# Optimization experiments

Hardware: AMD Instinct MI355X
Metric: run time of the kernel (lower is better)

The kernel has to match this reference:

```python
import jax, jax.numpy as jnp
import numpy as np

INPUT_DIM = 6
HIDDEN = 256
NUM_CLASSES = 8
B = 16
V = 32768


def setup_inputs() -> dict:
    key = jax.random.key(0)
    ks = jax.random.split(key, 8)
    x = jax.random.normal(ks[0], (B, INPUT_DIM, V), dtype=jnp.float32)
    obj_idx = jax.random.randint(ks[1], (B,), 0, NUM_CLASSES)
    # Stacked per-class expert weights (Conv1d kernel_size=1 == pointwise linear)
    s1 = 1.0 / np.sqrt(INPUT_DIM)
    s2 = 1.0 / np.sqrt(HIDDEN)
    w1 = jax.random.uniform(ks[2], (NUM_CLASSES, HIDDEN, INPUT_DIM), jnp.float32, -s1, s1)
    b1 = jax.random.uniform(ks[3], (NUM_CLASSES, HIDDEN), jnp.float32, -s1, s1)
    w2 = jax.random.uniform(ks[4], (NUM_CLASSES, HIDDEN, HIDDEN), jnp.float32, -s2, s2)
    b2 = jax.random.uniform(ks[5], (NUM_CLASSES, HIDDEN), jnp.float32, -s2, s2)
    w3 = jax.random.uniform(ks[6], (NUM_CLASSES, 1, HIDDEN), jnp.float32, -s2, s2)
    b3 = jax.random.uniform(ks[7], (NUM_CLASSES, 1), jnp.float32, -s2, s2)
    return {"x": x, "obj_idx": obj_idx, "w1": w1, "b1": b1,
            "w2": w2, "b2": b2, "w3": w3, "b3": b3}


def reference(x, obj_idx, w1, b1, w2, b2, w3, b3):
    # Gather each sample's expert weights, then run the fused 3-layer pointwise
    # MLP over all B*V positions in one batched einsum per layer (no Python
    # loop over samples, unlike the original torch code).
    # x: [B, 6, V] -> out: [B, 1, V]
    h = jax.nn.relu(jnp.einsum('boi,biv->bov', w1[obj_idx], x) + b1[obj_idx][:, :, None])
    h = jax.nn.relu(jnp.einsum('boi,biv->bov', w2[obj_idx], h) + b2[obj_idx][:, :, None])
    out = jnp.einsum('boi,biv->bov', w3[obj_idx], h) + b3[obj_idx][:, :, None]
    return out
```

## Files before the change

kernel.cpp:

```cpp
#include <hip/hip_runtime.h>
#include <hip/hip_bf16.h>

typedef __bf16 bf16x8 __attribute__((ext_vector_type(8)));
typedef __bf16 bf16x4 __attribute__((ext_vector_type(4)));
typedef float  f32x4  __attribute__((ext_vector_type(4)));
typedef float  f32x16 __attribute__((ext_vector_type(16)));

#define V_TOTAL 32768
#define NT      512
#define NV      32
#define NBLK    256

#define W2_LDS  32768
#define H1_LDS  65536
#define RED_LDS 4096
#define LDS_TOT (W2_LDS + H1_LDS + RED_LDS)

#define GLOAD_LDS16(g, l) __builtin_amdgcn_global_load_lds( \
    (const __attribute__((address_space(1))) void*)(g),     \
    (__attribute__((address_space(3))) void*)(l), 16, 0, 0)

__global__ void w2_to_bf16(const float* __restrict__ w2, __bf16* __restrict__ w2b) {
    int i = blockIdx.x * 256 + threadIdx.x;
    int e = i >> 16, q = i & 65535;
    int c = q >> 9, w = q & 511, lane = w >> 3, j = w & 7;
    int ks = c >> 3, tile = c & 7;
    int m = tile * 32 + (lane & 31);
    int k = ks * 16 + (lane >> 5) * 8 + j;
    w2b[i] = (__bf16)w2[e * 65536 + m * 256 + k];
}

__global__ __launch_bounds__(NT) void fused_mlp(
    const float* __restrict__ x,  const int* __restrict__ obj,
    const float* __restrict__ w1, const float* __restrict__ b1,
    const float* __restrict__ b2, const float* __restrict__ w3,
    const float* __restrict__ b3, const __bf16* __restrict__ w2b,
    float* __restrict__ out)
{
    extern __shared__ __align__(16) char smem[];
    char*  w2s = smem;
    char*  h1t = smem + W2_LDS;
    float* red = (float*)(smem + W2_LDS + H1_LDS);

    const int t    = threadIdx.x;
    const int lane = t & 63;
    const int wv   = t >> 6;
    const int c32  = lane & 31;
    const int hh   = lane >> 5;
    const int b    = blockIdx.x >> 4;
    const int g    = blockIdx.x & 15;
    const int e    = __builtin_amdgcn_readfirstlane(obj[b]);
    const __bf16* w2sw = w2b + (size_t)e * 65536;

    #pragma unroll
    for (int it = 0; it < 4; ++it) {
        int c0 = it * 8 + wv;
        GLOAD_LDS16(w2sw + c0 * 512 + lane * 8, w2s + c0 * 1024);
    }

    bf16x8 aar[12];
    #pragma unroll
    for (int k2 = 0; k2 < 12; ++k2)
        aar[k2] = *(const bf16x8*)(w2sw + ((4 + k2) * 8 + wv) * 512 + lane * 8);

    const float* w1e = w1 + e * 1536;
    const float* b1e = b1 + e * 256;
    const float* b2e = b2 + e * 256;
    const float* w3e = w3 + e * 256;
    bf16x8 aa1 = {};
    if (hh == 0)
        #pragma unroll
        for (int j = 0; j < 6; ++j) aa1[j] = (__bf16)w1e[(wv * 32 + c32) * 6 + j];
    const float b3e = b3[e];
    const float* xe = x + (size_t)b * 6 * V_TOTAL;

    bf16x8 xf[2];
    auto load_x = [&](int ic) {
        #pragma unroll
        for (int pt = 0; pt < 2; ++pt) {
            bf16x8 v = {};
            #pragma unroll
            for (int i = 0; i < 6; ++i)
                v[i] = (__bf16)xe[i * V_TOTAL + (g * NV + ic) * 64 + pt * 32 + c32];
            xf[pt] = v;
        }
    };
    auto do_l1 = [&](int pan) {
        f32x16 b1f;
        #pragma unroll
        for (int gg = 0; gg < 4; ++gg) {
            f32x4 v = *(const f32x4*)(b1e + wv * 32 + gg * 8 + hh * 4);
            #pragma unroll
            for (int q = 0; q < 4; ++q) b1f[gg * 4 + q] = v[q];
        }
        #pragma unroll
        for (int pt = 0; pt < 2; ++pt) {
            f32x16 h = __builtin_amdgcn_mfma_f32_32x32x16_bf16(aa1, xf[pt], b1f, 0, 0, 0);
            #pragma unroll
            for (int gg = 0; gg < 4; ++gg) {
                bf16x4 pk;
                #pragma unroll
                for (int q = 0; q < 4; ++q) pk[q] = (__bf16)fmaxf(h[gg * 4 + q], 0.f);
                *(bf16x4*)(h1t + pan * 32768 + ((wv * 2 + (gg >> 1)) * 2 + pt) * 1024
                           + (gg & 1) * 512 + c32 * 16 + hh * 8) = pk;
            }
        }
    };

    load_x(0);
    do_l1(0);
    load_x(1);

    for (int iv = 0; iv < NV; ++iv) {
        __syncthreads();

        if (iv > 0 && t < 64) {
            const float* rq = red + ((iv - 1) & 1) * 512;
            float s = b3e;
            #pragma unroll
            for (int w8 = 0; w8 < 8; ++w8) s += rq[w8 * 64 + t];
            out[(size_t)b * V_TOTAL + (g * NV + iv - 1) * 64 + t] = s;
        }

        f32x16 acc0, acc1;
        #pragma unroll
        for (int gg = 0; gg < 4; ++gg) {
            f32x4 v = *(const f32x4*)(b2e + wv * 32 + gg * 8 + hh * 4);
            #pragma unroll
            for (int q = 0; q < 4; ++q) { acc0[gg * 4 + q] = v[q]; acc1[gg * 4 + q] = v[q]; }
        }
        const char* bbase = h1t + (iv & 1) * 32768 + lane * 16;
        #pragma unroll
        for (int ks = 0; ks < 4; ++ks) {
            const bf16x8 aw = *(const bf16x8*)(w2s + (ks * 8 + wv) * 1024 + lane * 16);
            const bf16x8 bb0 = *(const bf16x8*)(bbase + (ks * 2 + 0) * 1024);
            const bf16x8 bb1 = *(const bf16x8*)(bbase + (ks * 2 + 1) * 1024);
            acc0 = __builtin_amdgcn_mfma_f32_32x32x16_bf16(aw, bb0, acc0, 0, 0, 0);
            acc1 = __builtin_amdgcn_mfma_f32_32x32x16_bf16(aw, bb1, acc1, 0, 0, 0);
        }
        #pragma unroll
        for (int k2 = 0; k2 < 12; ++k2) {
            const bf16x8 bb0 = *(const bf16x8*)(bbase + ((4 + k2) * 2 + 0) * 1024);
            const bf16x8 bb1 = *(const bf16x8*)(bbase + ((4 + k2) * 2 + 1) * 1024);
            acc0 = __builtin_amdgcn_mfma_f32_32x32x16_bf16(aar[k2], bb0, acc0, 0, 0, 0);
            acc1 = __builtin_amdgcn_mfma_f32_32x32x16_bf16(aar[k2], bb1, acc1, 0, 0, 0);
        }

        float p0 = 0.f, p1 = 0.f;
        #pragma unroll
        for (int gg = 0; gg < 4; ++gg) {
            f32x4 wq = *(const f32x4*)(w3e + wv * 32 + gg * 8 + hh * 4);
            #pragma unroll
            for (int q = 0; q < 4; ++q) {
                p0 = fmaf(wq[q], fmaxf(acc0[gg * 4 + q], 0.f), p0);
                p1 = fmaf(wq[q], fmaxf(acc1[gg * 4 + q], 0.f), p1);
            }
        }
        p0 += __shfl_xor(p0, 32, 64);
        p1 += __shfl_xor(p1, 32, 64);
        float* rp = red + (iv & 1) * 512;
        if (lane < 32) {
            rp[wv * 64 + c32]      = p0;
            rp[wv * 64 + 32 + c32] = p1;
        }

        if (iv + 1 < NV) {
            do_l1((iv + 1) & 1);
            if (iv + 2 < NV) load_x(iv + 2);
        }
    }
    __syncthreads();
    if (t < 64) {
        const float* rq = red + ((NV - 1) & 1) * 512;
        float s = b3e;
        #pragma unroll
        for (int w8 = 0; w8 < 8; ++w8) s += rq[w8 * 64 + t];
        out[(size_t)b * V_TOTAL + (g * NV + NV - 1) * 64 + t] = s;
    }
}

extern "C" void kernel_launch(void* const* d_in, const int* in_sizes, int n_in,
                              void* d_out, int out_size, void* d_ws, size_t ws_size,
                              hipStream_t stream) {
    const float* x   = (const float*)d_in[0];
    const int*   obj = (const int*)d_in[1];
    const float* w1  = (const float*)d_in[2];
    const float* b1  = (const float*)d_in[3];
    const float* w2  = (const float*)d_in[4];
    const float* b2  = (const float*)d_in[5];
    const float* w3  = (const float*)d_in[6];
    const float* b3  = (const float*)d_in[7];
    float*  out = (float*)d_out;
    __bf16* w2b = (__bf16*)d_ws;

    (void)hipFuncSetAttribute((const void*)fused_mlp,
                              hipFuncAttributeMaxDynamicSharedMemorySize, LDS_TOT);

    w2_to_bf16<<<2048, 256, 0, stream>>>(w2, w2b);
    fused_mlp<<<NBLK, NT, LDS_TOT, stream>>>(x, obj, w1, b1, b2, w3, b3, w2b, out);
}
```

Baseline: 76.11 us.

## Add producer warps for layer-1 and move more W2 into LDS

Raises the block to 10 waves: eight consumer waves run the layer-2 MFMA and layer-3 reduction, and two new producer waves load x, compute layer 1 into the double-buffered LDS panel, and write the final output. Half of W2 now sits in LDS (64KB) and half in registers, down from 12 register fragments to 8. The goal is to take layer-1 work and x loads off the critical MFMA waves and lower their register pressure. In exchange, each producer wave now runs 8 layer-1 MFMAs per step and reloads w1/b1 from global memory, which may make the producers the bottleneck.

Measured after the change: 117.9 us. +54.9%, slower.

```diff
diff --git a/kernel.cpp b/kernel.cpp
--- a/kernel.cpp
+++ b/kernel.cpp
@@ -7,11 +7,11 @@
 typedef float  f32x16 __attribute__((ext_vector_type(16)));
 
 #define V_TOTAL 32768
-#define NT      512
+#define NT      640
 #define NV      32
 #define NBLK    256
 
-#define W2_LDS  32768
+#define W2_LDS  65536
 #define H1_LDS  65536
 #define RED_LDS 4096
 #define LDS_TOT (W2_LDS + H1_LDS + RED_LDS)
@@ -51,131 +51,124 @@
     const int g    = blockIdx.x & 15;
     const int e    = __builtin_amdgcn_readfirstlane(obj[b]);
     const __bf16* w2sw = w2b + (size_t)e * 65536;
+    const int p    = wv - 8;
 
-    #pragma unroll
-    for (int it = 0; it < 4; ++it) {
-        int c0 = it * 8 + wv;
-        GLOAD_LDS16(w2sw + c0 * 512 + lane * 8, w2s + c0 * 1024);
+    if (wv < 8) {
+        #pragma unroll
+        for (int it = 0; it < 8; ++it) {
+            int c0 = it * 8 + wv;
+            GLOAD_LDS16(w2sw + c0 * 512 + lane * 8, w2s + c0 * 1024);
+        }
     }
-
-    bf16x8 aar[12];
-    #pragma unroll
-    for (int k2 = 0; k2 < 12; ++k2)
-        aar[k2] = *(const bf16x8*)(w2sw + ((4 + k2) * 8 + wv) * 512 + lane * 8);
 
     const float* w1e = w1 + e * 1536;
     const float* b1e = b1 + e * 256;
     const float* b2e = b2 + e * 256;
     const float* w3e = w3 + e * 256;
-    bf16x8 aa1 = {};
-    if (hh == 0)
-        #pragma unroll
-        for (int j = 0; j < 6; ++j) aa1[j] = (__bf16)w1e[(wv * 32 + c32) * 6 + j];
-    const float b3e = b3[e];
+    const float  b3e = b3[e];
     const float* xe = x + (size_t)b * 6 * V_TOTAL;
 
-    bf16x8 xf[2];
-    auto load_x = [&](int ic) {
+    bf16x8 aar[8];
+    if (wv < 8)
         #pragma unroll
-        for (int pt = 0; pt < 2; ++pt) {
-            bf16x8 v = {};
+        for (int k2 = 0; k2 < 8; ++k2)
+            aar[k2] = *(const bf16x8*)(w2sw + ((8 + k2) * 8 + wv) * 512 + lane * 8);
+
+    auto produce = [&](int icb, int pan) {
+        bf16x8 xfp = {};
+        #pragma unroll
+        for (int i = 0; i < 6; ++i)
+            xfp[i] = (__bf16)xe[i * V_TOTAL + (g * NV + icb) * 64 + p * 32 + c32];
+        #pragma unroll
+        for (int tile = 0; tile < 8; ++tile) {
+            bf16x8 a1 = {};
+            if (hh == 0)
+                #pragma unroll
+                for (int j = 0; j < 6; ++j)
+                    a1[j] = (__bf16)w1e[(tile * 32 + c32) * 6 + j];
+            f32x16 b1f;
             #pragma unroll
-            for (int i = 0; i < 6; ++i)
-                v[i] = (__bf16)xe[i * V_TOTAL + (g * NV + ic) * 64 + pt * 32 + c32];
-            xf[pt] = v;
-        }
-    };
-    auto do_l1 = [&](int pan) {
-        f32x16 b1f;
-        #pragma unroll
-        for (int gg = 0; gg < 4; ++gg) {
-            f32x4 v = *(const f32x4*)(b1e + wv * 32 + gg * 8 + hh * 4);
-            #pragma unroll
-            for (int q = 0; q < 4; ++q) b1f[gg * 4 + q] = v[q];
-        }
-        #pragma unroll
-        for (int pt = 0; pt < 2; ++pt) {
-            f32x16 h = __builtin_amdgcn_mfma_f32_32x32x16_bf16(aa1, xf[pt], b1f, 0, 0, 0);
+            for (int gg = 0; gg < 4; ++gg) {
+                f32x4 v = *(const f32x4*)(b1e + tile * 32 + gg * 8 + hh * 4);
+                #pragma unroll
+                for (int q = 0; q < 4; ++q) b1f[gg * 4 + q] = v[q];
+            }
+            f32x16 h = __builtin_amdgcn_mfma_f32_32x32x16_bf16(a1, xfp, b1f, 0, 0, 0);
             #pragma unroll
             for (int gg = 0; gg < 4; ++gg) {
                 bf16x4 pk;
                 #pragma unroll
                 for (int q = 0; q < 4; ++q) pk[q] = (__bf16)fmaxf(h[gg * 4 + q], 0.f);
-                *(bf16x4*)(h1t + pan * 32768 + ((wv * 2 + (gg >> 1)) * 2 + pt) * 1024
+                *(bf16x4*)(h1t + pan * 32768 + ((tile * 2 + (gg >> 1)) * 2 + p) * 1024
                            + (gg & 1) * 512 + c32 * 16 + hh * 8) = pk;
             }
         }
     };
 
-    load_x(0);
-    do_l1(0);
-    load_x(1);
+    if (wv >= 8) produce(0, 0);
 
     for (int iv = 0; iv < NV; ++iv) {
         __syncthreads();
 
-        if (iv > 0 && t < 64) {
-            const float* rq = red + ((iv - 1) & 1) * 512;
-            float s = b3e;
+        if (wv < 8) {
+            f32x16 acc0, acc1;
             #pragma unroll
-            for (int w8 = 0; w8 < 8; ++w8) s += rq[w8 * 64 + t];
-            out[(size_t)b * V_TOTAL + (g * NV + iv - 1) * 64 + t] = s;
-        }
-
-        f32x16 acc0, acc1;
-        #pragma unroll
-        for (int gg = 0; gg < 4; ++gg) {
-            f32x4 v = *(const f32x4*)(b2e + wv * 32 + gg * 8 + hh * 4);
+            for (int gg = 0; gg < 4; ++gg) {
+                f32x4 v = *(const f32x4*)(b2e + wv * 32 + gg * 8 + hh * 4);
+                #pragma unroll
+                for (int q = 0; q < 4; ++q) { acc0[gg*4+q] = v[q]; acc1[gg*4+q] = v[q]; }
+            }
+            const char* bbase = h1t + (iv & 1) * 32768 + lane * 16;
             #pragma unroll
-            for (int q = 0; q < 4; ++q) { acc0[gg * 4 + q] = v[q]; acc1[gg * 4 + q] = v[q]; }
-        }
-        const char* bbase = h1t + (iv & 1) * 32768 + lane * 16;
-        #pragma unroll
-        for (int ks = 0; ks < 4; ++ks) {
-            const bf16x8 aw = *(const bf16x8*)(w2s + (ks * 8 + wv) * 1024 + lane * 16);
-            const bf16x8 bb0 = *(const bf16x8*)(bbase + (ks * 2 + 0) * 1024);
-            const bf16x8 bb1 = *(const bf16x8*)(bbase + (ks * 2 + 1) * 1024);
-            acc0 = __builtin_amdgcn_mfma_f32_32x32x16_bf16(aw, bb0, acc0, 0, 0, 0);
-            acc1 = __builtin_amdgcn_mfma_f32_32x32x16_bf16(aw, bb1, acc1, 0, 0, 0);
-        }
-        #pragma unroll
-        for (int k2 = 0; k2 < 12; ++k2) {
-            const bf16x8 bb0 = *(const bf16x8*)(bbase + ((4 + k2) * 2 + 0) * 1024);
-            const bf16x8 bb1 = *(const bf16x8*)(bbase + ((4 + k2) * 2 + 1) * 1024);
-            acc0 = __builtin_amdgcn_mfma_f32_32x32x16_bf16(aar[k2], bb0, acc0, 0, 0, 0);
-            acc1 = __builtin_amdgcn_mfma_f32_32x32x16_bf16(aar[k2], bb1, acc1, 0, 0, 0);
-        }
-
-        float p0 = 0.f, p1 = 0.f;
-        #pragma unroll
-        for (int gg = 0; gg < 4; ++gg) {
-            f32x4 wq = *(const f32x4*)(w3e + wv * 32 + gg * 8 + hh * 4);
+            for (int ks = 0; ks < 8; ++ks) {
+                const bf16x8 aw  = *(const bf16x8*)(w2s + (ks * 8 + wv) * 1024 + lane * 16);
+                const bf16x8 bb0 = *(const bf16x8*)(bbase + (ks * 2 + 0) * 1024);
+                const bf16x8 bb1 = *(const bf16x8*)(bbase + (ks * 2 + 1) * 1024);
+                acc0 = __builtin_amdgcn_mfma_f32_32x32x16_bf16(aw, bb0, acc0, 0, 0, 0);
+                acc1 = __builtin_amdgcn_mfma_f32_32x32x16_bf16(aw, bb1, acc1, 0, 0, 0);
+            }
             #pragma unroll
-            for (int q = 0; q < 4; ++q) {
-                p0 = fmaf(wq[q], fmaxf(acc0[gg * 4 + q], 0.f), p0);
-                p1 = fmaf(wq[q], fmaxf(acc1[gg * 4 + q], 0.f), p1);
+            for (int k2 = 0; k2 < 8; ++k2) {
+                const bf16x8 bb0 = *(const bf16x8*)(bbase + ((8 + k2) * 2 + 0) * 1024);
+                const bf16x8 bb1 = *(const bf16x8*)(bbase + ((8 + k2) * 2 + 1) * 1024);
+                acc0 = __builtin_amdgcn_mfma_f32_32x32x16_bf16(aar[k2], bb0, acc0, 0, 0, 0);
+                acc1 = __builtin_amdgcn_mfma_f32_32x32x16_bf16(aar[k2], bb1, acc1, 0, 0, 0);
             }
-        }
-        p0 += __shfl_xor(p0, 32, 64);
-        p1 += __shfl_xor(p1, 32, 64);
-        float* rp = red + (iv & 1) * 512;
-        if (lane < 32) {
-            rp[wv * 64 + c32]      = p0;
-            rp[wv * 64 + 32 + c32] = p1;
-        }
-
-        if (iv + 1 < NV) {
-            do_l1((iv + 1) & 1);
-            if (iv + 2 < NV) load_x(iv + 2);
+            float p0 = 0.f, p1 = 0.f;
+            #pragma unroll
+            for (int gg = 0; gg < 4; ++gg) {
+                f32x4 wq = *(const f32x4*)(w3e + wv * 32 + gg * 8 + hh * 4);
+                #pragma unroll
+                for (int q = 0; q < 4; ++q) {
+                    p0 = fmaf(wq[q], fmaxf(acc0[gg * 4 + q], 0.f), p0);
+                    p1 = fmaf(wq[q], fmaxf(acc1[gg * 4 + q], 0.f), p1);
+                }
+            }
+            p0 += __shfl_xor(p0, 32, 64);
+            p1 += __shfl_xor(p1, 32, 64);
+            float* rp = red + (iv & 1) * 512;
+            if (lane < 32) {
+                rp[wv * 64 + c32]      = p0;
+                rp[wv * 64 + 32 + c32] = p1;
+            }
+        } else {
+            if (p == 0 && iv > 0) {
+                const float* rq = red + ((iv - 1) & 1) * 512;
+                float s = b3e;
+                #pragma unroll
+                for (int w8 = 0; w8 < 8; ++w8) s += rq[w8 * 64 + lane];
+                out[(size_t)b * V_TOTAL + (g * NV + iv - 1) * 64 + lane] = s;
+            }
+            if (iv + 1 < NV) produce(iv + 1, (iv + 1) & 1);
         }
     }
     __syncthreads();
-    if (t < 64) {
+    if (wv == 8) {
         const float* rq = red + ((NV - 1) & 1) * 512;
         float s = b3e;
         #pragma unroll
-        for (int w8 = 0; w8 < 8; ++w8) s += rq[w8 * 64 + t];
-        out[(size_t)b * V_TOTAL + (g * NV + NV - 1) * 64 + t] = s;
+        for (int w8 = 0; w8 < 8; ++w8) s += rq[w8 * 64 + lane];
+        out[(size_t)b * V_TOTAL + (g * NV + NV - 1) * 64 + lane] = s;
     }
 }
 
```
